# Optimization experiments

Measured on AMD Instinct MI355X. Metric: run time of the kernel, lower is better.

Reference implementation:

```python
import jax, jax.numpy as jnp
import numpy as np

HID = 128
N_LAYERS = 4
IN_DIM = 2


def _gru_layer(x_seq, W_ih, W_hh, b_ih, b_hh):
    """PyTorch-equivalent single GRU layer.
    x_seq: (T, N, F); W_ih: (3H, F); W_hh: (3H, H); b_ih, b_hh: (3H,)
    Gate order (PyTorch): r, z, n.
    """
    T, N, _ = x_seq.shape
    # precompute input projections for all timesteps: (T, N, 3H)
    gi = jnp.einsum('tnf,gf->tng', x_seq, W_ih) + b_ih

    def step(h, gi_t):
        gh = h @ W_hh.T + b_hh                      # (N, 3H)
        gi_r, gi_z, gi_n = jnp.split(gi_t, 3, axis=-1)
        gh_r, gh_z, gh_n = jnp.split(gh, 3, axis=-1)
        r = jax.nn.sigmoid(gi_r + gh_r)
        z = jax.nn.sigmoid(gi_z + gh_z)
        n = jnp.tanh(gi_n + r * gh_n)
        h_new = (1.0 - z) * n + z * h
        return h_new, h_new

    h0 = jnp.zeros((N, HID), dtype=x_seq.dtype)
    _, out = jax.lax.scan(step, h0, gi)
    return out                                       # (T, N, H)


def setup_inputs() -> dict:
    key = jax.random.key(0)
    ks = jax.random.split(key, 12)
    s = 1.0 / np.sqrt(HID)  # PyTorch GRU init scale
    x = jax.random.normal(ks[0], (512, IN_DIM, 1024), dtype=jnp.float32)
    W_ih0 = jax.random.uniform(ks[1], (3 * HID, IN_DIM), minval=-s, maxval=s)
    W_ih_rest = jax.random.uniform(ks[2], (N_LAYERS - 1, 3 * HID, HID), minval=-s, maxval=s)
    W_hh = jax.random.uniform(ks[3], (N_LAYERS, 3 * HID, HID), minval=-s, maxval=s)
    b_ih = jax.random.uniform(ks[4], (N_LAYERS, 3 * HID), minval=-s, maxval=s)
    b_hh = jax.random.uniform(ks[5], (N_LAYERS, 3 * HID), minval=-s, maxval=s)
    fc1_w = jax.random.uniform(ks[6], (HID, HID), minval=-s, maxval=s)
    fc1_b = jax.random.uniform(ks[7], (HID,), minval=-s, maxval=s)
    fc2_w = jax.random.uniform(ks[8], (3, HID), minval=-s, maxval=s)
    fc2_b = jax.random.uniform(ks[9], (3,), minval=-s, maxval=s)
    return {"x": x, "W_ih0": W_ih0, "W_ih_rest": W_ih_rest, "W_hh": W_hh,
            "b_ih": b_ih, "b_hh": b_hh, "fc1_w": fc1_w, "fc1_b": fc1_b,
            "fc2_w": fc2_w, "fc2_b": fc2_b}


def reference(x, W_ih0, W_ih_rest, W_hh, b_ih, b_hh, fc1_w, fc1_b, fc2_w, fc2_b):
    # x: (B, 2, S) -> transpose(1,2) -> (B, S, 2); GRU (batch_first=False)
    # treats axis0 as time T=B, axis1 as batch N=S.
    h = jnp.transpose(x, (0, 2, 1))                  # (T, N, 2)
    h = _gru_layer(h, W_ih0, W_hh[0], b_ih[0], b_hh[0])
    for l in range(1, N_LAYERS):
        h = _gru_layer(h, W_ih_rest[l - 1], W_hh[l], b_ih[l], b_hh[l])
    # out[:, -1, :] -> last lane along the GRU batch axis: (T, H)
    last = h[:, -1, :]
    hidden = jax.nn.relu(last @ fc1_w.T + fc1_b)
    return hidden @ fc2_w.T + fc2_b                  # (B, 3)
```

## Files before the change

### kernel.cpp

```cpp
#include <hip/hip_runtime.h>
#include <math.h>

#define T_SEQ  512
#define HID    128
#define G3     384
#define NL     4
#define CHUNK  8
#define NCHUNK (T_SEQ / CHUNK)

#define GI_TOT   (NL * T_SEQ * G3)
#define SEQ_TOT  (NL * T_SEQ * HID)
#define FLAG_OFF (GI_TOT + SEQ_TOT)

__device__ __forceinline__ float fsig(float x) {
    float e = __expf(-x);
    return 1.0f / (1.0f + e);
}
__device__ __forceinline__ float ftanh(float x) {
    float ax = fabsf(x);
    float e = __expf(-2.0f * ax);
    float t = (1.0f - e) / (1.0f + e);
    return copysignf(t, x);
}
__device__ __forceinline__ float rdlane(float v, int k) {
    return __uint_as_float(__builtin_amdgcn_readlane(__float_as_uint(v), k));
}


__global__ void init_flags(int* fl) {
    int i = threadIdx.x;
    if (i < 8) fl[i * 16] = (i == 0) ? NCHUNK : 0;
}

__global__ void gi0_kernel(const float* __restrict__ x, const float* __restrict__ Wih0,
                           const float* __restrict__ bih, float* __restrict__ gi) {
    int t = blockIdx.x;
    int g = threadIdx.x;
    float x0 = x[t * 2048 + 1023];
    float x1 = x[t * 2048 + 1024 + 1023];
    gi[t * G3 + g] = bih[g] + Wih0[g * 2 + 0] * x0 + Wih0[g * 2 + 1] * x1;
}

__global__ __launch_bounds__(256, 1) void pipe_kernel(float* __restrict__ ws,
                                                      const float* __restrict__ WihR,
                                                      const float* __restrict__ bih,
                                                      const float* __restrict__ Whh,
                                                      const float* __restrict__ bhh) {
    __shared__ float smem[12288];

    int bid  = blockIdx.x;
    int tid  = threadIdx.x;
    int lane = tid & 63;
    int q    = tid >> 6;
    int row0 = lane * 6;
    int* fl = (int*)(ws + FLAG_OFF);
    bool is_rec = (bid & 1) == 0;
    int  l      = is_rec ? (bid >> 1) : ((bid + 1) >> 1);

    if (is_rec) {
        const float* W   = Whh + (size_t)l * G3 * HID;
        const float* gi  = ws + (size_t)l * T_SEQ * G3;
        float* seq_o     = ws + GI_TOT + (size_t)l * T_SEQ * HID;
        float* aux       = smem + 3072;
        int* in_flag     = &fl[l * 16];
        int* out_flag    = &fl[(4 + l) * 16];

        float w[6][32];
        const float* wbase = W + q * 32;
#pragma unroll
        for (int i = 0; i < 6; i++) {
            const float4* wr = reinterpret_cast<const float4*>(wbase + (size_t)(row0 + i) * HID);
#pragma unroll
            for (int c = 0; c < 8; c++) {
                float4 v = wr[c];
                w[i][c * 4 + 0] = v.x; w[i][c * 4 + 1] = v.y;
                w[i][c * 4 + 2] = v.z; w[i][c * 4 + 3] = v.w;
            }
        }

        int  m  = lane & 31;
        bool p2 = (lane < 32);
        int  j  = q * 32 + m;
        const float* bb = bhh + (size_t)l * G3;
        float br = 0.f, bz = 0.f, bn = 0.f;
        if (p2) { br = bb[j]; bz = bb[HID + j]; bn = bb[2 * HID + j]; }

        float hs[32];
#pragma unroll
        for (int k = 0; k < 32; k++) hs[k] = 0.f;
        float hprev = 0.f;
        float g_r[CHUNK], g_z[CHUNK], g_n[CHUNK];

        for (int c = 0; c < NCHUNK; c++) {
            if (tid == 0) {
                while (__hip_atomic_fetch_add(in_flag, 0, __ATOMIC_RELAXED, __HIP_MEMORY_SCOPE_AGENT) < c + 1)
                    __builtin_amdgcn_s_sleep(2);
            }
            __syncthreads();
            int t0 = c * CHUNK;
            if (p2) {
                const float* gp = gi + (size_t)t0 * G3 + j;
#pragma unroll
                for (int s = 0; s < CHUNK; s++) {
                    g_r[s] = gp[s * G3];
                    g_z[s] = gp[s * G3 + HID];
                    g_n[s] = gp[s * G3 + 2 * HID];
                }
            }
#pragma unroll
            for (int s = 0; s < CHUNK; s++) {
                int t = t0 + s;
                float* psb = smem + (t & 1) * 1536;
                float acc[6];
#pragma unroll
                for (int i = 0; i < 6; i++) {
                    float a0 = 0.f, a1 = 0.f, a2 = 0.f, a3 = 0.f;
#pragma unroll
                    for (int k = 0; k < 32; k += 4) {
                        a0 += w[i][k]     * hs[k];
                        a1 += w[i][k + 1] * hs[k + 1];
                        a2 += w[i][k + 2] * hs[k + 2];
                        a3 += w[i][k + 3] * hs[k + 3];
                    }
                    acc[i] = (a0 + a1) + (a2 + a3);
                }
#pragma unroll
                for (int i = 0; i < 6; i += 2) {
                    float2 p; p.x = acc[i]; p.y = acc[i + 1];
                    *reinterpret_cast<float2*>(&psb[q * G3 + row0 + i]) = p;
                }
                __syncthreads();
                float hn_bc = 0.f;
                if (p2) {
                    float ghr = (psb[j]         + psb[G3 + j])         + (psb[2*G3 + j]         + psb[3*G3 + j]);
                    float ghz = (psb[HID + j]   + psb[G3 + HID + j])   + (psb[2*G3 + HID + j]   + psb[3*G3 + HID + j]);
                    float ghn = (psb[2*HID + j] + psb[G3 + 2*HID + j]) + (psb[2*G3 + 2*HID + j] + psb[3*G3 + 2*HID + j]);
                    float r = fsig(g_r[s] + ghr + br);
                    float z = fsig(g_z[s] + ghz + bz);
                    float n = ftanh(g_n[s] + r * (ghn + bn));
                    float hn = (1.0f - z) * n + z * hprev;
                    hprev = hn;
                    aux[s * HID + j] = hn;
                    hn_bc = hn;
                }
#pragma unroll
                for (int k = 0; k < 32; k++) hs[k] = rdlane(hn_bc, k);
            }
            __syncthreads();
            {
                float4 v = *reinterpret_cast<const float4*>(&aux[tid * 4]);
                *reinterpret_cast<float4*>(&seq_o[(size_t)t0 * HID + tid * 4]) = v;
            }
            __syncthreads();
            if (tid == 0)
                __hip_atomic_store(out_flag, c + 1, __ATOMIC_RELEASE, __HIP_MEMORY_SCOPE_AGENT);
        }
    } else {
        const float* W   = WihR + (size_t)(l - 1) * G3 * HID;
        const float* seq_in = ws + GI_TOT + (size_t)(l - 1) * T_SEQ * HID;
        float* gi_o      = ws + (size_t)l * T_SEQ * G3;
        int* in_flag     = &fl[(4 + (l - 1)) * 16];
        int* out_flag    = &fl[l * 16];

        float w[6][32];
        const float* wbase = W + q * 32;
#pragma unroll
        for (int i = 0; i < 6; i++) {
            const float4* wr = reinterpret_cast<const float4*>(wbase + (size_t)(row0 + i) * HID);
#pragma unroll
            for (int c = 0; c < 8; c++) {
                float4 v = wr[c];
                w[i][c * 4 + 0] = v.x; w[i][c * 4 + 1] = v.y;
                w[i][c * 4 + 2] = v.z; w[i][c * 4 + 3] = v.w;
            }
        }
        int m  = lane & 31;
        int m2 = tid & 31;
        int s2 = tid >> 5;
        const float* bb = bih + (size_t)l * G3;
        float br4[4], bz4[4], bn4[4];
#pragma unroll
        for (int u = 0; u < 4; u++) {
            int jj = u * 32 + m2;
            br4[u] = bb[jj]; bz4[u] = bb[HID + jj]; bn4[u] = bb[2 * HID + jj];
        }

        for (int c = 0; c < NCHUNK; c++) {
            if (tid == 0) {
                while (__hip_atomic_fetch_add(in_flag, 0, __ATOMIC_RELAXED, __HIP_MEMORY_SCOPE_AGENT) < c + 1)
                    __builtin_amdgcn_s_sleep(2);
            }
            __syncthreads();
            int t0 = c * CHUNK;
            float vseq[CHUNK];
            {
                const float* sp = seq_in + (size_t)t0 * HID + q * 32 + m;
#pragma unroll
                for (int s = 0; s < CHUNK; s++) vseq[s] = sp[s * HID];
            }
#pragma unroll
            for (int s = 0; s < CHUNK; s++) {
                float xs[32];
#pragma unroll
                for (int k = 0; k < 32; k++) xs[k] = rdlane(vseq[s], k);
                float acc[6];
#pragma unroll
                for (int i = 0; i < 6; i++) {
                    float a0 = 0.f, a1 = 0.f, a2 = 0.f, a3 = 0.f;
#pragma unroll
                    for (int k = 0; k < 32; k += 4) {
                        a0 += w[i][k]     * xs[k];
                        a1 += w[i][k + 1] * xs[k + 1];
                        a2 += w[i][k + 2] * xs[k + 2];
                        a3 += w[i][k + 3] * xs[k + 3];
                    }
                    acc[i] = (a0 + a1) + (a2 + a3);
                }
                float* pp = smem + s * 1536;
#pragma unroll
                for (int i = 0; i < 6; i += 2) {
                    float2 p; p.x = acc[i]; p.y = acc[i + 1];
                    *reinterpret_cast<float2*>(&pp[q * G3 + row0 + i]) = p;
                }
            }
            __syncthreads();
#pragma unroll
            for (int u = 0; u < 4; u++) {
                int jj = u * 32 + m2;
                const float* pp = smem + s2 * 1536;
                float vr = (pp[jj]         + pp[G3 + jj])         + (pp[2*G3 + jj]         + pp[3*G3 + jj]);
                float vz = (pp[HID + jj]   + pp[G3 + HID + jj])   + (pp[2*G3 + HID + jj]   + pp[3*G3 + HID + jj]);
                float vn = (pp[2*HID + jj] + pp[G3 + 2*HID + jj]) + (pp[2*G3 + 2*HID + jj] + pp[3*G3 + 2*HID + jj]);
                float* gp = gi_o + (size_t)(t0 + s2) * G3;
                gp[jj]           = vr + br4[u];
                gp[HID + jj]     = vz + bz4[u];
                gp[2 * HID + jj] = vn + bn4[u];
            }
            __syncthreads();
            if (tid == 0)
                __hip_atomic_store(out_flag, c + 1, __ATOMIC_RELEASE, __HIP_MEMORY_SCOPE_AGENT);
        }
    }
}

__global__ void fc_kernel(const float* __restrict__ seq, const float* __restrict__ fc1w,
                          const float* __restrict__ fc1b, const float* __restrict__ fc2w,
                          const float* __restrict__ fc2b, float* __restrict__ out) {
    __shared__ float h3[HID];
    __shared__ float hid[HID];
    int t = blockIdx.x;
    int i = threadIdx.x;
    h3[i] = seq[t * HID + i];
    __syncthreads();
    const float4* w4 = reinterpret_cast<const float4*>(fc1w + i * HID);
    const float4* h4 = reinterpret_cast<const float4*>(h3);
    float a0 = 0.f, a1 = 0.f, a2 = 0.f, a3 = 0.f;
#pragma unroll
    for (int k = 0; k < 32; k += 4) {
        float4 w0 = w4[k], w1 = w4[k + 1], w2 = w4[k + 2], w3 = w4[k + 3];
        float4 h0 = h4[k], h1 = h4[k + 1], h2 = h4[k + 2], h3v = h4[k + 3];
        a0 += w0.x * h0.x + w0.y * h0.y + w0.z * h0.z + w0.w * h0.w;
        a1 += w1.x * h1.x + w1.y * h1.y + w1.z * h1.z + w1.w * h1.w;
        a2 += w2.x * h2.x + w2.y * h2.y + w2.z * h2.z + w2.w * h2.w;
        a3 += w3.x * h3v.x + w3.y * h3v.y + w3.z * h3v.z + w3.w * h3v.w;
    }
    float v = fc1b[i] + ((a0 + a1) + (a2 + a3));
    hid[i] = v > 0.0f ? v : 0.0f;
    __syncthreads();
    if (i < 3) {
        const float* w = fc2w + i * HID;
        float s = 0.f;
#pragma unroll
        for (int k = 0; k < HID; k++) s += w[k] * hid[k];
        out[t * 3 + i] = fc2b[i] + s;
    }
}

extern "C" void kernel_launch(void* const* d_in, const int* in_sizes, int n_in,
                              void* d_out, int out_size, void* d_ws, size_t ws_size,
                              hipStream_t stream) {
    const float* x     = (const float*)d_in[0];
    const float* Wih0  = (const float*)d_in[1];
    const float* WihR  = (const float*)d_in[2];
    const float* Whh   = (const float*)d_in[3];
    const float* bih   = (const float*)d_in[4];
    const float* bhh   = (const float*)d_in[5];
    const float* fc1w  = (const float*)d_in[6];
    const float* fc1b  = (const float*)d_in[7];
    const float* fc2w  = (const float*)d_in[8];
    const float* fc2b  = (const float*)d_in[9];
    float* out = (float*)d_out;
    float* ws  = (float*)d_ws;

    int*   flags = (int*)(ws + FLAG_OFF);
    float* gi0   = ws;
    float* seq3  = ws + GI_TOT + (size_t)3 * T_SEQ * HID;

    init_flags<<<1, 64, 0, stream>>>(flags);
    gi0_kernel<<<T_SEQ, G3, 0, stream>>>(x, Wih0, bih, gi0);
    pipe_kernel<<<7, 256, 0, stream>>>(ws, WihR, bih, Whh, bhh);
    fc_kernel<<<T_SEQ, HID, 0, stream>>>(seq3, fc1w, fc1b, fc2w, fc2b, out);
}
```

Baseline: 394.0 us.

## Prefetch next chunk's input gates and poll flag mid-chunk in recurrent GRU loop

The recurrent layer loop now polls the producer flag inside the timestep loop of the current chunk and loads the next chunk's input-gate values into registers partway through it. This takes the flag spin, the barrier and the global load latency off the critical path at each chunk boundary. The hidden-state dot product is also rewritten with float2 vector arithmetic, aiming for packed FMA instructions. The cost is higher register pressure from the extra prefetch buffers, and the next chunk's loads rely on the flag seen at step 3 with no __syncthreads before the load at step 4 other than the existing per-step barrier.

```diff
diff --git a/kernel.cpp b/kernel.cpp
--- a/kernel.cpp
+++ b/kernel.cpp
@@ -90,39 +90,45 @@
         for (int k = 0; k < 32; k++) hs[k] = 0.f;
         float hprev = 0.f;
         float g_r[CHUNK], g_z[CHUNK], g_n[CHUNK];
+        float n_r[CHUNK], n_z[CHUNK], n_n[CHUNK];
+        int   fseen = 0;
+
+        if (tid == 0) {
+            while (__hip_atomic_fetch_add(in_flag, 0, __ATOMIC_RELAXED, __HIP_MEMORY_SCOPE_AGENT) < 1)
+                __builtin_amdgcn_s_sleep(2);
+        }
+        __syncthreads();
+        if (p2) {
+            const float* gp = gi + j;
+#pragma unroll
+            for (int s = 0; s < CHUNK; s++) {
+                g_r[s] = gp[s * G3];
+                g_z[s] = gp[s * G3 + HID];
+                g_n[s] = gp[s * G3 + 2 * HID];
+            }
+        }
 
         for (int c = 0; c < NCHUNK; c++) {
-            if (tid == 0) {
-                while (__hip_atomic_fetch_add(in_flag, 0, __ATOMIC_RELAXED, __HIP_MEMORY_SCOPE_AGENT) < c + 1)
-                    __builtin_amdgcn_s_sleep(2);
-            }
-            __syncthreads();
             int t0 = c * CHUNK;
-            if (p2) {
-                const float* gp = gi + (size_t)t0 * G3 + j;
-#pragma unroll
-                for (int s = 0; s < CHUNK; s++) {
-                    g_r[s] = gp[s * G3];
-                    g_z[s] = gp[s * G3 + HID];
-                    g_n[s] = gp[s * G3 + 2 * HID];
-                }
-            }
+            bool more = (c + 1 < NCHUNK);
 #pragma unroll
             for (int s = 0; s < CHUNK; s++) {
                 int t = t0 + s;
                 float* psb = smem + (t & 1) * 1536;
+                float2 hs2[16];
+#pragma unroll
+                for (int k = 0; k < 16; k++) { hs2[k].x = hs[2 * k]; hs2[k].y = hs[2 * k + 1]; }
                 float acc[6];
 #pragma unroll
                 for (int i = 0; i < 6; i++) {
-                    float a0 = 0.f, a1 = 0.f, a2 = 0.f, a3 = 0.f;
-#pragma unroll
-                    for (int k = 0; k < 32; k += 4) {
-                        a0 += w[i][k]     * hs[k];
-                        a1 += w[i][k + 1] * hs[k + 1];
-                        a2 += w[i][k + 2] * hs[k + 2];
-                        a3 += w[i][k + 3] * hs[k + 3];
+                    const float2* w2 = reinterpret_cast<const float2*>(w[i]);
+                    float2 s0 = {0.f, 0.f}, s1 = {0.f, 0.f};
+#pragma unroll
+                    for (int k = 0; k < 16; k += 2) {
+                        s0 += w2[k]     * hs2[k];
+                        s1 += w2[k + 1] * hs2[k + 1];
                     }
-                    acc[i] = (a0 + a1) + (a2 + a3);
+                    acc[i] = (s0.x + s0.y) + (s1.x + s1.y);
                 }
 #pragma unroll
                 for (int i = 0; i < 6; i += 2) {
@@ -130,6 +136,15 @@
                     *reinterpret_cast<float2*>(&psb[q * G3 + row0 + i]) = p;
                 }
                 __syncthreads();
+                if (s == 4 && more && p2) {
+                    const float* gp = gi + (size_t)(t0 + CHUNK) * G3 + j;
+#pragma unroll
+                    for (int u = 0; u < CHUNK; u++) {
+                        n_r[u] = gp[u * G3];
+                        n_z[u] = gp[u * G3 + HID];
+                        n_n[u] = gp[u * G3 + 2 * HID];
+                    }
+                }
                 float hn_bc = 0.f;
                 if (p2) {
                     float ghr = (psb[j]         + psb[G3 + j])         + (psb[2*G3 + j]         + psb[3*G3 + j]);
@@ -143,6 +158,14 @@
                     aux[s * HID + j] = hn;
                     hn_bc = hn;
                 }
+                if (s == 2 && more && tid == 0)
+                    fseen = __hip_atomic_fetch_add(in_flag, 0, __ATOMIC_RELAXED, __HIP_MEMORY_SCOPE_AGENT);
+                if (s == 3 && more && tid == 0) {
+                    while (fseen < c + 2) {
+                        __builtin_amdgcn_s_sleep(2);
+                        fseen = __hip_atomic_fetch_add(in_flag, 0, __ATOMIC_RELAXED, __HIP_MEMORY_SCOPE_AGENT);
+                    }
+                }
 #pragma unroll
                 for (int k = 0; k < 32; k++) hs[k] = rdlane(hn_bc, k);
             }
@@ -154,6 +177,12 @@
             __syncthreads();
             if (tid == 0)
                 __hip_atomic_store(out_flag, c + 1, __ATOMIC_RELEASE, __HIP_MEMORY_SCOPE_AGENT);
+            if (more) {
+#pragma unroll
+                for (int u = 0; u < CHUNK; u++) {
+                    g_r[u] = n_r[u]; g_z[u] = n_z[u]; g_n[u] = n_n[u];
+                }
+            }
         }
     } else {
         const float* W   = WihR + (size_t)(l - 1) * G3 * HID;
```

After: 437.9 us. 1.11x slower.
